# Optimization experiments

Hardware: AMD Instinct MI355X
Metric: run time of the kernel (lower is better)

The kernel has to match this reference:

```python
import jax, jax.numpy as jnp
import numpy as np

N = 100000
E = 3200000
IN_DIM, HID, MLP_HID, K = 3, 64, 128, 15


def setup_inputs() -> dict:
    key = jax.random.key(0)
    ks = jax.random.split(key, 10)
    x = jax.random.normal(ks[0], (N, IN_DIM), dtype=jnp.float32)
    edge_index = jax.random.randint(ks[1], (2, E), 0, N, dtype=jnp.int32)
    def glorot(k, shape):
        lim = float(np.sqrt(6.0 / (shape[0] + shape[1])))
        return jax.random.uniform(k, shape, jnp.float32, -lim, lim)
    return {
        "x": x,
        "edge_index": edge_index,
        "W1": glorot(ks[2], (IN_DIM, HID)), "b1": jnp.zeros((HID,), jnp.float32),
        "W2": glorot(ks[3], (HID, HID)),    "b2": jnp.zeros((HID,), jnp.float32),
        "Wm1": glorot(ks[4], (HID, MLP_HID)), "bm1": jnp.zeros((MLP_HID,), jnp.float32),
        "Wm2": glorot(ks[5], (MLP_HID, K)),   "bm2": jnp.zeros((K,), jnp.float32),
    }


def _gcn_layer(h, W, b, src, dst, deg_inv_sqrt, n):
    # h: [N, Fin] -> [N, Fout]; GCNConv: D^-1/2 (A+I) D^-1/2 (h W) + b
    hw = h @ W  # dense GEMM first (Fin small)
    norm = deg_inv_sqrt[src] * deg_inv_sqrt[dst]  # [E+N]
    msg = hw[src] * norm[:, None]                 # irregular gather, [E+N, Fout]
    out = jax.ops.segment_sum(msg, dst, num_segments=n)  # scatter-add
    return out + b


def reference(x, edge_index, W1, b1, W2, b2, Wm1, bm1, Wm2, bm2):
    n = x.shape[0]
    loops = jnp.arange(n, dtype=edge_index.dtype)
    src = jnp.concatenate([edge_index[0], loops])  # self-loops appended
    dst = jnp.concatenate([edge_index[1], loops])
    deg = jax.ops.segment_sum(jnp.ones_like(dst, dtype=x.dtype), dst, num_segments=n)
    deg_inv_sqrt = jnp.where(deg > 0, jax.lax.rsqrt(jnp.maximum(deg, 1.0)), 0.0)

    h = jax.nn.elu(_gcn_layer(x, W1, b1, src, dst, deg_inv_sqrt, n))
    h = jax.nn.elu(_gcn_layer(h, W2, b2, src, dst, deg_inv_sqrt, n))
    # MLP (dropout is identity in eval mode)
    h = jax.nn.elu(h @ Wm1 + bm1)
    H = h @ Wm2 + bm2
    return jax.nn.softmax(H, axis=1)  # [N, K]
```

## Files before the change

kernel.cpp:

```cpp
#include <hip/hip_runtime.h>
#include <hip/hip_fp16.h>
#include <math.h>


#define SPAN 128
#define CAP  4608
#define CH   8192
#define EPT  16
#define H2P  88
#define MSP2 136

typedef _Float16 v8hf __attribute__((ext_vector_type(8)));
typedef float    v4f  __attribute__((ext_vector_type(4)));

__device__ __forceinline__ float elu(float v) { return v > 0.f ? v : expm1f(v); }

__global__ __launch_bounds__(512) void scatter_kernel(const int* __restrict__ src,
    const int* __restrict__ dst, int* __restrict__ cursor, unsigned* __restrict__ colb,
    const float* __restrict__ W2, const float* __restrict__ Wm1,
    const float* __restrict__ Wm2, __half* __restrict__ W2t,
    __half* __restrict__ Wm1t, __half* __restrict__ Wm2p,
    int E, int NBK, int nChunks) {
    int tid = threadIdx.x;
    if ((int)blockIdx.x == nChunks) {
        for (int i = tid; i < 64 * 64; i += 512) {
            int f = i >> 6, k = i & 63;
            W2t[f * 64 + k] = __float2half(W2[k * 64 + f]);
        }
        for (int i = tid; i < 128 * 64; i += 512) {
            int j = i >> 6, f = i & 63;
            Wm1t[j * 64 + f] = __float2half(Wm1[f * 128 + j]);
        }
        for (int i = tid; i < 4 * 64 * 8; i += 512) {
            int j = i & 7, l = (i >> 3) & 63, t = i >> 9;
            int k = t * 32 + (l >> 4) * 8 + j;
            int c = l & 15;
            Wm2p[i] = (c < 15) ? __float2half(Wm2[k * 15 + c]) : __half(0.f);
        }
        return;
    }
    __shared__ int hist[1024];
    __shared__ unsigned gb[1024];
    int chunk = blockIdx.x;
    for (int i = tid; i < NBK; i += 512) hist[i] = 0;
    __syncthreads();
    int base = chunk * CH;
    int cnt = min(CH, E - base);
    unsigned br[EPT], dt[EPT];
#pragma unroll
    for (int j = 0; j < EPT; ++j) {
        int idx = j * 512 + tid;
        br[j] = 0xFFFFFFFFu;
        if (idx < cnt) {
            int e = base + idx;
            int s = src[e], d = dst[e];
            int b = d >> 7;
            int r = atomicAdd(&hist[b], 1);
            br[j] = ((unsigned)b << 13) | (unsigned)r;
            dt[j] = ((unsigned)(d & 127) << 17) | (unsigned)s;
        }
    }
    __syncthreads();
    for (int b = tid; b < NBK; b += 512) {
        int c = hist[b];
        gb[b] = (unsigned)(b * CAP) + (c ? (unsigned)atomicAdd(&cursor[b], c) : 0u);
    }
    __syncthreads();
#pragma unroll
    for (int j = 0; j < EPT; ++j) {
        if (br[j] != 0xFFFFFFFFu) {
            int b = br[j] >> 13;
            int r = br[j] & 8191;
            unsigned pos = gb[b] + (unsigned)r;
            if (pos < (unsigned)(b + 1) * CAP) colb[pos] = dt[j];
        }
    }
}

__global__ __launch_bounds__(512) void csr_sort_kernel(unsigned* __restrict__ colb,
    const int* __restrict__ cursor, const float* __restrict__ x,
    uint2* __restrict__ rp2, float* __restrict__ dis, __half* __restrict__ sxh,
    int N) {
    __shared__ __align__(16) unsigned ebuf[CAP];
    __shared__ __align__(16) int sbuf[CAP];
    __shared__ int cnt[SPAN], pref[SPAN], fill[SPAN];
    int b = blockIdx.x, tid = threadIdx.x;
    int n = min(cursor[b], CAP);
    size_t base = (size_t)b * CAP;
    if (tid < SPAN) cnt[tid] = 0;
    int n4 = n >> 2;
    for (int k = tid; k < n4; k += 512)
        *(uint4*)(ebuf + 4 * k) = *(const uint4*)(colb + base + 4 * k);
    for (int i = (n4 << 2) + tid; i < n; i += 512) ebuf[i] = colb[base + i];
    __syncthreads();
    for (int i = tid; i < n; i += 512) atomicAdd(&cnt[(ebuf[i] >> 17) & 127], 1);
    __syncthreads();
    if (tid < SPAN) pref[tid] = cnt[tid];
    __syncthreads();
    for (int off = 1; off < SPAN; off <<= 1) {
        int xv = (tid < SPAN && tid >= off) ? pref[tid - off] : 0;
        __syncthreads();
        if (tid < SPAN) pref[tid] += xv;
        __syncthreads();
    }
    if (tid < SPAN) {
        int ex = pref[tid] - cnt[tid];
        fill[tid] = ex;
        int node = b * SPAN + tid;
        if (node < N) {
            uint2 rp;
            rp.x = (unsigned)(base + ex);
            rp.y = (unsigned)(base + ex + cnt[tid]);
            rp2[node] = rp;
            float r = rsqrtf((float)(cnt[tid] + 1));
            dis[node] = r;
            __half2 h0 = __floats2half2_rn(r * x[node * 3 + 0], r * x[node * 3 + 1]);
            __half2 h1 = __floats2half2_rn(r * x[node * 3 + 2], 0.f);
            uint2 w; w.x = *(unsigned*)&h0; w.y = *(unsigned*)&h1;
            *(uint2*)(sxh + (size_t)node * 4) = w;
        }
    }
    __syncthreads();
    for (int i = tid; i < n; i += 512) {
        unsigned e = ebuf[i];
        int pos = atomicAdd(&fill[(e >> 17) & 127], 1);
        sbuf[pos] = (int)(e & 0x1FFFF);
    }
    __syncthreads();
    for (int k = tid; k < n4; k += 512)
        *(uint4*)(colb + base + 4 * k) = *(const uint4*)(sbuf + 4 * k);
    for (int i = (n4 << 2) + tid; i < n; i += 512) colb[base + i] = (unsigned)sbuf[i];
}

__global__ void agg3_kernel(const __half* __restrict__ sxh, const uint2* __restrict__ rp2,
                            const unsigned* __restrict__ colb, const float* __restrict__ dis,
                            const float* __restrict__ W1, const float* __restrict__ b1,
                            __half* __restrict__ s1h, int N) {
    int wave = (blockIdx.x * blockDim.x + threadIdx.x) >> 6;
    int lane = threadIdx.x & 63;
    int hl = lane & 31;
    int d = wave * 2 + (lane >> 5);
    bool act = d < N;
    int start = 0, end = 0;
    if (act) { uint2 rp = rp2[d]; start = (int)rp.x; end = (int)rp.y; }
    float a0 = 0.f, a1 = 0.f, a2v = 0.f;
    for (int i = start + hl; i < end; i += 32) {
        uint2 rq = *(const uint2*)(sxh + (size_t)colb[i] * 4);
        float2 u0 = __half22float2(*(__half2*)&rq.x);
        float2 u1 = __half22float2(*(__half2*)&rq.y);
        a0 += u0.x; a1 += u0.y; a2v += u1.x;
    }
#pragma unroll
    for (int off = 16; off; off >>= 1) {
        a0  += __shfl_xor(a0, off);
        a1  += __shfl_xor(a1, off);
        a2v += __shfl_xor(a2v, off);
    }
    if (act) {
        uint2 rq = *(const uint2*)(sxh + (size_t)d * 4);
        float2 u0 = __half22float2(*(__half2*)&rq.x);
        float2 u1 = __half22float2(*(__half2*)&rq.y);
        a0 += u0.x; a1 += u0.y; a2v += u1.x;
        float r = dis[d];
        float v0 = r * (a0 * W1[hl]      + a1 * W1[64 + hl]      + a2v * W1[128 + hl])      + b1[hl];
        float v1 = r * (a0 * W1[32 + hl] + a1 * W1[96 + hl]      + a2v * W1[160 + hl])      + b1[32 + hl];
        s1h[(size_t)d * 64 + hl]      = __float2half(r * elu(v0));
        s1h[(size_t)d * 64 + 32 + hl] = __float2half(r * elu(v1));
    }
}

__global__ void agg64_kernel(const __half2* __restrict__ s1h, const uint2* __restrict__ rp2,
                             const unsigned* __restrict__ colb, const float* __restrict__ dis,
                             __half2* __restrict__ a2h, int N) {
    int wave = (blockIdx.x * blockDim.x + threadIdx.x) >> 6;
    int lane = threadIdx.x & 63;
    int hl = lane & 31;
    int d = wave * 2 + (lane >> 5);
    bool act = d < N;
    int start = 0, end = 0;
    if (act) { uint2 rp = rp2[d]; start = (int)rp.x; end = (int)rp.y; }
    float a0x = 0.f, a0y = 0.f, a1x = 0.f, a1y = 0.f;
    float a2x = 0.f, a2y = 0.f, a3x = 0.f, a3y = 0.f;
    if (act) {
        float2 v = __half22float2(s1h[(size_t)d * 32 + hl]);
        a0x = v.x; a0y = v.y;
    }
    int i = start;
    for (; i + 7 < end; i += 8) {
        int c0 = (int)colb[i],     c1 = (int)colb[i + 1];
        int c2 = (int)colb[i + 2], c3 = (int)colb[i + 3];
        int c4 = (int)colb[i + 4], c5 = (int)colb[i + 5];
        int c6 = (int)colb[i + 6], c7 = (int)colb[i + 7];
        __half2 v0 = s1h[(size_t)c0 * 32 + hl];
        __half2 v1 = s1h[(size_t)c1 * 32 + hl];
        __half2 v2 = s1h[(size_t)c2 * 32 + hl];
        __half2 v3 = s1h[(size_t)c3 * 32 + hl];
        __half2 v4 = s1h[(size_t)c4 * 32 + hl];
        __half2 v5 = s1h[(size_t)c5 * 32 + hl];
        __half2 v6 = s1h[(size_t)c6 * 32 + hl];
        __half2 v7 = s1h[(size_t)c7 * 32 + hl];
        float2 p0 = __half22float2(__hadd2(v0, v1));
        float2 p1 = __half22float2(__hadd2(v2, v3));
        float2 p2 = __half22float2(__hadd2(v4, v5));
        float2 p3 = __half22float2(__hadd2(v6, v7));
        a0x += p0.x; a0y += p0.y; a1x += p1.x; a1y += p1.y;
        a2x += p2.x; a2y += p2.y; a3x += p3.x; a3y += p3.y;
    }
    for (; i < end; ++i) {
        float2 v = __half22float2(s1h[(size_t)colb[i] * 32 + hl]);
        a0x += v.x; a0y += v.y;
    }
    if (act) {
        float r = dis[d];
        float ox = r * ((a0x + a1x) + (a2x + a3x));
        float oy = r * ((a0y + a1y) + (a2y + a3y));
        a2h[(size_t)d * 32 + hl] = __floats2half2_rn(ox, oy);
    }
}

__global__ __launch_bounds__(256) void h1_kernel(const __half* __restrict__ a2h,
    const __half* __restrict__ W2t, const float* __restrict__ b2g,
    const __half* __restrict__ Wm1t, const float* __restrict__ bm1g,
    const __half* __restrict__ Wm2p, const float* __restrict__ bm2g,
    float* __restrict__ out, int N) {
    __shared__ __align__(16) __half h2s[64 * H2P];
    __shared__ __align__(16) __half ms[64 * MSP2];
    int tid = threadIdx.x;
    int wave = tid >> 6, lane = tid & 63;
    int q = lane >> 4, l16 = lane & 15;
    int base = blockIdx.x * 64;

    v8hf wc[4];
#pragma unroll
    for (int t = 0; t < 4; ++t)
        wc[t] = *(const v8hf*)(Wm2p + ((size_t)(t * 64 + lane)) * 8);
    float bbc = (l16 < 15) ? bm2g[l16] : 0.f;

    {
        int nodeRow = base + wave * 16 + l16;
        size_t arow = (size_t)min(nodeRow, N - 1) * 64;
        v8hf af0 = *(const v8hf*)(a2h + arow + q * 8);
        v8hf af1 = *(const v8hf*)(a2h + arow + 32 + q * 8);
#pragma unroll
        for (int fb = 0; fb < 4; ++fb) {
            float bb = b2g[fb * 16 + l16];
            v4f acc = {bb, bb, bb, bb};
            v8hf b0 = *(const v8hf*)(W2t + (fb * 16 + l16) * 64 + q * 8);
            v8hf b1 = *(const v8hf*)(W2t + (fb * 16 + l16) * 64 + 32 + q * 8);
            acc = __builtin_amdgcn_mfma_f32_16x16x32_f16(af0, b0, acc, 0, 0, 0);
            acc = __builtin_amdgcn_mfma_f32_16x16x32_f16(af1, b1, acc, 0, 0, 0);
#pragma unroll
            for (int r = 0; r < 4; ++r)
                h2s[(wave * 16 + q * 4 + r) * H2P + fb * 16 + l16] =
                    __float2half(elu(acc[r]));
        }
    }
    __syncthreads();
    {
        int arow = (wave * 16 + l16) * H2P;
        v8hf af0 = *(const v8hf*)(h2s + arow + q * 8);
        v8hf af1 = *(const v8hf*)(h2s + arow + 32 + q * 8);
#pragma unroll
        for (int jb = 0; jb < 8; ++jb) {
            float bb = bm1g[jb * 16 + l16];
            v4f acc = {bb, bb, bb, bb};
            v8hf b0 = *(const v8hf*)(Wm1t + (jb * 16 + l16) * 64 + q * 8);
            v8hf b1 = *(const v8hf*)(Wm1t + (jb * 16 + l16) * 64 + 32 + q * 8);
            acc = __builtin_amdgcn_mfma_f32_16x16x32_f16(af0, b0, acc, 0, 0, 0);
            acc = __builtin_amdgcn_mfma_f32_16x16x32_f16(af1, b1, acc, 0, 0, 0);
#pragma unroll
            for (int r = 0; r < 4; ++r)
                ms[(wave * 16 + q * 4 + r) * MSP2 + jb * 16 + l16] =
                    __float2half(elu(acc[r]));
        }
    }
    __syncthreads();
    {
        int arow = (wave * 16 + l16) * MSP2;
        v4f accC = {bbc, bbc, bbc, bbc};
#pragma unroll
        for (int t = 0; t < 4; ++t) {
            v8hf a = *(const v8hf*)(ms + arow + t * 32 + q * 8);
            accC = __builtin_amdgcn_mfma_f32_16x16x32_f16(a, wc[t], accC, 0, 0, 0);
        }
#pragma unroll
        for (int r = 0; r < 4; ++r) {
            float lg = (l16 < 15) ? accC[r] : -1e30f;
            float mx = lg;
            mx = fmaxf(mx, __shfl_xor(mx, 1));
            mx = fmaxf(mx, __shfl_xor(mx, 2));
            mx = fmaxf(mx, __shfl_xor(mx, 4));
            mx = fmaxf(mx, __shfl_xor(mx, 8));
            float ex = (l16 < 15) ? __expf(lg - mx) : 0.f;
            float sden = ex;
            sden += __shfl_xor(sden, 1);
            sden += __shfl_xor(sden, 2);
            sden += __shfl_xor(sden, 4);
            sden += __shfl_xor(sden, 8);
            int node = base + wave * 16 + q * 4 + r;
            if (l16 < 15 && node < N)
                out[(size_t)node * 15 + l16] = ex / sden;
        }
    }
}

extern "C" void kernel_launch(void* const* d_in, const int* in_sizes, int n_in,
                              void* d_out, int out_size, void* d_ws, size_t ws_size,
                              hipStream_t stream) {
    const float* x   = (const float*)d_in[0];
    const int*   ei  = (const int*)d_in[1];
    const float* W1  = (const float*)d_in[2];
    const float* b1  = (const float*)d_in[3];
    const float* W2  = (const float*)d_in[4];
    const float* b2  = (const float*)d_in[5];
    const float* Wm1 = (const float*)d_in[6];
    const float* bm1 = (const float*)d_in[7];
    const float* Wm2 = (const float*)d_in[8];
    const float* bm2 = (const float*)d_in[9];
    float* out = (float*)d_out;

    int N = in_sizes[0] / 3;
    int E = in_sizes[1] / 2;
    const int* src = ei;
    const int* dst = ei + E;
    int NBK = (N + SPAN - 1) / SPAN;

    uintptr_t p = (uintptr_t)d_ws;
    auto carve = [&](size_t bytes) -> void* {
        p = (p + 255) & ~(uintptr_t)255;
        void* r = (void*)p;
        p += bytes;
        return r;
    };
    unsigned* colb    = (unsigned*)carve((size_t)NBK * CAP * 4);
    __half*   a2h     = (__half*)carve((size_t)N * 64 * 2);
    __half*   s1h     = (__half*)carve((size_t)N * 64 * 2);
    int*      cursor  = (int*)carve((size_t)NBK * 4);
    uint2*    rp2     = (uint2*)carve((size_t)N * 8);
    float*    dis     = (float*)carve((size_t)N * 4);
    __half*   sxh     = (__half*)carve((size_t)N * 8);
    __half*   W2t     = (__half*)carve(64 * 64 * 2);
    __half*   Wm1t    = (__half*)carve(128 * 64 * 2);
    __half*   Wm2p    = (__half*)carve(4 * 64 * 8 * 2);

    int nChunks = (E + CH - 1) / CH;
    int aggBlocks = (N + 7) / 8;
    int nTiles = (N + 63) / 64;

    hipMemsetAsync(cursor, 0, (size_t)NBK * 4, stream);
    scatter_kernel<<<nChunks + 1, 512, 0, stream>>>(src, dst, cursor, colb,
        W2, Wm1, Wm2, W2t, Wm1t, Wm2p, E, NBK, nChunks);
    csr_sort_kernel<<<NBK, 512, 0, stream>>>(colb, cursor, x, rp2, dis, sxh, N);
    agg3_kernel<<<aggBlocks, 256, 0, stream>>>(sxh, rp2, colb, dis, W1, b1, s1h, N);
    agg64_kernel<<<aggBlocks, 256, 0, stream>>>((const __half2*)s1h, rp2, colb, dis,
                                                (__half2*)a2h, N);
    h1_kernel<<<nTiles, 256, 0, stream>>>(a2h, W2t, b2, Wm1t, bm1, Wm2p, bm2, out, N);
}
```

Measured before the change: 241.0 us.

## Restructure 64-wide aggregation: one wave per node, 8 edges in parallel with 16-byte gathers

The second-layer aggregation changes from two nodes per wave, each half-wave walking edges one at a time with 4-byte loads, to one node per wave. Each group of 8 lanes handles one edge and loads a full 128-byte row as 16-byte vectors, two edges per iteration, then combines groups with cross-lane shuffle reductions. The aim is fewer serial loop iterations per node and wider memory transactions for the irregular gather. In exchange it adds shuffle reduction overhead and wasted lanes for low-degree nodes, and the colb buffer gets padding because reads can run past the end of the edge list.

```diff
diff --git a/kernel.cpp b/kernel.cpp
--- a/kernel.cpp
+++ b/kernel.cpp
@@ -169,52 +169,68 @@
     }
 }
 
-__global__ void agg64_kernel(const __half2* __restrict__ s1h, const uint2* __restrict__ rp2,
+__global__ void agg64_kernel(const __half* __restrict__ s1h, const uint2* __restrict__ rp2,
                              const unsigned* __restrict__ colb, const float* __restrict__ dis,
-                             __half2* __restrict__ a2h, int N) {
+                             __half* __restrict__ a2h, int N) {
     int wave = (blockIdx.x * blockDim.x + threadIdx.x) >> 6;
     int lane = threadIdx.x & 63;
-    int hl = lane & 31;
-    int d = wave * 2 + (lane >> 5);
-    bool act = d < N;
-    int start = 0, end = 0;
-    if (act) { uint2 rp = rp2[d]; start = (int)rp.x; end = (int)rp.y; }
-    float a0x = 0.f, a0y = 0.f, a1x = 0.f, a1y = 0.f;
-    float a2x = 0.f, a2y = 0.f, a3x = 0.f, a3y = 0.f;
-    if (act) {
-        float2 v = __half22float2(s1h[(size_t)d * 32 + hl]);
-        a0x = v.x; a0y = v.y;
-    }
-    int i = start;
-    for (; i + 7 < end; i += 8) {
-        int c0 = (int)colb[i],     c1 = (int)colb[i + 1];
-        int c2 = (int)colb[i + 2], c3 = (int)colb[i + 3];
-        int c4 = (int)colb[i + 4], c5 = (int)colb[i + 5];
-        int c6 = (int)colb[i + 6], c7 = (int)colb[i + 7];
-        __half2 v0 = s1h[(size_t)c0 * 32 + hl];
-        __half2 v1 = s1h[(size_t)c1 * 32 + hl];
-        __half2 v2 = s1h[(size_t)c2 * 32 + hl];
-        __half2 v3 = s1h[(size_t)c3 * 32 + hl];
-        __half2 v4 = s1h[(size_t)c4 * 32 + hl];
-        __half2 v5 = s1h[(size_t)c5 * 32 + hl];
-        __half2 v6 = s1h[(size_t)c6 * 32 + hl];
-        __half2 v7 = s1h[(size_t)c7 * 32 + hl];
-        float2 p0 = __half22float2(__hadd2(v0, v1));
-        float2 p1 = __half22float2(__hadd2(v2, v3));
-        float2 p2 = __half22float2(__hadd2(v4, v5));
-        float2 p3 = __half22float2(__hadd2(v6, v7));
-        a0x += p0.x; a0y += p0.y; a1x += p1.x; a1y += p1.y;
-        a2x += p2.x; a2y += p2.y; a3x += p3.x; a3y += p3.y;
-    }
-    for (; i < end; ++i) {
-        float2 v = __half22float2(s1h[(size_t)colb[i] * 32 + hl]);
-        a0x += v.x; a0y += v.y;
-    }
-    if (act) {
-        float r = dis[d];
-        float ox = r * ((a0x + a1x) + (a2x + a3x));
-        float oy = r * ((a0y + a1y) + (a2y + a3y));
-        a2h[(size_t)d * 32 + hl] = __floats2half2_rn(ox, oy);
+    int g = lane >> 3;
+    int f = lane & 7;
+    int d = wave;
+    if (d >= N) return;
+    uint2 rp = rp2[d];
+    int start = (int)rp.x;
+    int ne = (int)(rp.y - rp.x);
+    int nslots = ne + 1;
+    int npair = (nslots + 15) >> 4;
+    float acc0 = 0.f, acc1 = 0.f, acc2 = 0.f, acc3 = 0.f;
+    float acc4 = 0.f, acc5 = 0.f, acc6 = 0.f, acc7 = 0.f;
+    for (int p = 0; p < npair; ++p) {
+        int ja = p * 16 + g;
+        int jb = ja + 8;
+        int ca = (int)colb[start + ja];
+        int cb = (int)colb[start + jb];
+        bool oa = ja < nslots, ob = jb < nslots;
+        ca = (ja < ne) ? ca : d;
+        cb = (jb < ne) ? cb : d;
+        uint4 A = *(const uint4*)(s1h + (size_t)ca * 64 + f * 8);
+        uint4 B = *(const uint4*)(s1h + (size_t)cb * 64 + f * 8);
+        A.x = oa ? A.x : 0u; A.y = oa ? A.y : 0u;
+        A.z = oa ? A.z : 0u; A.w = oa ? A.w : 0u;
+        B.x = ob ? B.x : 0u; B.y = ob ? B.y : 0u;
+        B.z = ob ? B.z : 0u; B.w = ob ? B.w : 0u;
+        __half2 p0 = __hadd2(*(__half2*)&A.x, *(__half2*)&B.x);
+        __half2 p1 = __hadd2(*(__half2*)&A.y, *(__half2*)&B.y);
+        __half2 p2 = __hadd2(*(__half2*)&A.z, *(__half2*)&B.z);
+        __half2 p3 = __hadd2(*(__half2*)&A.w, *(__half2*)&B.w);
+        float2 q0 = __half22float2(p0);
+        float2 q1 = __half22float2(p1);
+        float2 q2 = __half22float2(p2);
+        float2 q3 = __half22float2(p3);
+        acc0 += q0.x; acc1 += q0.y; acc2 += q1.x; acc3 += q1.y;
+        acc4 += q2.x; acc5 += q2.y; acc6 += q3.x; acc7 += q3.y;
+    }
+#pragma unroll
+    for (int off = 8; off <= 32; off <<= 1) {
+        acc0 += __shfl_xor(acc0, off);
+        acc1 += __shfl_xor(acc1, off);
+        acc2 += __shfl_xor(acc2, off);
+        acc3 += __shfl_xor(acc3, off);
+        acc4 += __shfl_xor(acc4, off);
+        acc5 += __shfl_xor(acc5, off);
+        acc6 += __shfl_xor(acc6, off);
+        acc7 += __shfl_xor(acc7, off);
+    }
+    float r = dis[d];
+    if (g == 0) {
+        __half2 o0 = __floats2half2_rn(r * acc0, r * acc1);
+        __half2 o1 = __floats2half2_rn(r * acc2, r * acc3);
+        __half2 o2 = __floats2half2_rn(r * acc4, r * acc5);
+        __half2 o3 = __floats2half2_rn(r * acc6, r * acc7);
+        uint4 w;
+        w.x = *(unsigned*)&o0; w.y = *(unsigned*)&o1;
+        w.z = *(unsigned*)&o2; w.w = *(unsigned*)&o3;
+        *(uint4*)(a2h + (size_t)d * 64 + f * 8) = w;
     }
 }
 
@@ -332,7 +348,7 @@
         p += bytes;
         return r;
     };
-    unsigned* colb    = (unsigned*)carve((size_t)NBK * CAP * 4);
+    unsigned* colb    = (unsigned*)carve((size_t)NBK * CAP * 4 + 256);
     __half*   a2h     = (__half*)carve((size_t)N * 64 * 2);
     __half*   s1h     = (__half*)carve((size_t)N * 64 * 2);
     int*      cursor  = (int*)carve((size_t)NBK * 4);
@@ -345,6 +361,7 @@
 
     int nChunks = (E + CH - 1) / CH;
     int aggBlocks = (N + 7) / 8;
+    int aggBlocks64 = (N + 3) / 4;
     int nTiles = (N + 63) / 64;
 
     hipMemsetAsync(cursor, 0, (size_t)NBK * 4, stream);
@@ -352,7 +369,6 @@
         W2, Wm1, Wm2, W2t, Wm1t, Wm2p, E, NBK, nChunks);
     csr_sort_kernel<<<NBK, 512, 0, stream>>>(colb, cursor, x, rp2, dis, sxh, N);
     agg3_kernel<<<aggBlocks, 256, 0, stream>>>(sxh, rp2, colb, dis, W1, b1, s1h, N);
-    agg64_kernel<<<aggBlocks, 256, 0, stream>>>((const __half2*)s1h, rp2, colb, dis,
-                                                (__half2*)a2h, N);
+    agg64_kernel<<<aggBlocks64, 256, 0, stream>>>(s1h, rp2, colb, dis, a2h, N);
     h1_kernel<<<nTiles, 256, 0, stream>>>(a2h, W2t, b2, Wm1t, bm1, Wm2p, bm2, out, N);
 }
```

Result: faster. 233.0 us (-3.3%).
